# Kernel optimization log

Measured on AMD Instinct MI355X. Metric: run time of the kernel, lower is better.

The kernel has to match this reference:

```python
import jax, jax.numpy as jnp
import numpy as np

N, D, H, O, P = 50000, 256, 512, 64, 1024


def setup_inputs() -> dict:
    key = jax.random.key(0)
    ks = jax.random.split(key, 9)
    x = jax.random.normal(ks[0], (N, D), dtype=jnp.float32)
    W1 = jax.random.normal(ks[1], (H, D), dtype=jnp.float32) / np.sqrt(D)
    b1 = jax.random.normal(ks[2], (H,), dtype=jnp.float32) * 0.01
    W2 = jax.random.normal(ks[3], (O, H), dtype=jnp.float32) / np.sqrt(H)
    b2 = jax.random.normal(ks[4], (O,), dtype=jnp.float32) * 0.01
    ap = jax.random.randint(ks[5], (P,), 0, N, dtype=jnp.int32)
    p = jax.random.randint(ks[6], (P,), 0, N, dtype=jnp.int32)
    an = jax.random.randint(ks[7], (P,), 0, N, dtype=jnp.int32)
    n = jax.random.randint(ks[8], (P,), 0, N, dtype=jnp.int32)
    return {"x": x, "W1": W1, "b1": b1, "W2": W2, "b2": b2,
            "ap": ap, "p": p, "an": an, "n": n}


def reference(x, W1, b1, W2, b2, ap, p, an, n):
    """ContrastiveHessianCalculator.compute_hessian, loss_func='contrastive_full',
    wrt='weight', shape='diagonal', speed='half' (exact GGN diag), for the nnj net
    Linear(D,H) -> Tanh -> Linear(H,O).

    For a pair (x1,x2) the combined diag m0 - 2*m1 + m2 equals
    diag((J1-J2)^T (J1-J2)) where Ji = d f(xi)/d params. Closed form per layer:
      W1[i,j]: S11_i*x1_j^2 - 2*S12_i*x1_j*x2_j + S22_i*x2_j^2,
               Sab_i = tanh'(z1a)_i * tanh'(z1b)_i * sum_o W2[o,i]^2
      b1[i]:   S11_i - 2*S12_i + S22_i
      W2[i,j]: (h1_j - h2_j)^2  (independent of output row i)
      b2[i]:   0  (bias Jacobians of the two branches cancel)
    Per-layer diags are flattened [weight, bias] and concatenated (torch.cat(.., dim=1)),
    then summed over the pair batch; return sum(pos) - sum(neg).
    """
    c = jnp.sum(W2 * W2, axis=0)  # [H]

    def pair_hess_diag(ia, ib):
        xa = x[ia]            # [P, D]
        xb = x[ib]            # [P, D]
        ha = jnp.tanh(xa @ W1.T + b1)   # [P, H]
        hb = jnp.tanh(xb @ W1.T + b1)
        da = 1.0 - ha * ha              # tanh' at x_a, [P, H]
        db = 1.0 - hb * hb
        S11 = da * da * c               # [P, H]
        S12 = da * db * c
        S22 = db * db * c
        # W1 diag: [P, H, D]
        W1d = (S11[:, :, None] * (xa * xa)[:, None, :]
               - 2.0 * S12[:, :, None] * (xa * xb)[:, None, :]
               + S22[:, :, None] * (xb * xb)[:, None, :])
        b1d = S11 - 2.0 * S12 + S22      # [P, H]
        hd = (ha - hb) ** 2              # [P, H]
        W2d = jnp.broadcast_to(hd[:, None, :], (hd.shape[0], O, H))  # [P, O, H]
        b2d = jnp.zeros((hd.shape[0], O), dtype=hd.dtype)
        flat = jnp.concatenate([W1d.reshape(hd.shape[0], -1), b1d,
                                W2d.reshape(hd.shape[0], -1), b2d], axis=1)
        return jnp.sum(flat, axis=0)     # sum over pair batch -> [n_params]

    pos = pair_hess_diag(ap, p)
    neg = pair_hess_diag(an, n)
    return pos - neg
```

## Files before the change

### kernel.cpp

```cpp
#include <hip/hip_runtime.h>
#include <math.h>

#define DD_ 256
#define HH_ 512
#define OO_ 64

typedef __attribute__((ext_vector_type(8))) short bf16x8s;
typedef __attribute__((ext_vector_type(4))) float f32x4;

__device__ __forceinline__ unsigned short f2bf(float f) {
    unsigned u = __float_as_uint(f);
    u += 0x7FFF + ((u >> 16) & 1);
    return (unsigned short)(u >> 16);
}
__device__ __forceinline__ float bf2f(unsigned short h) {
    return __uint_as_float(((unsigned)h) << 16);
}
__device__ __forceinline__ int swz4(int r, int g) {
    return g ^ (r & 3) ^ ((r >> 2) & 3);
}

__global__ __launch_bounds__(256) void k_prep(
    const float* __restrict__ x, const float* __restrict__ W1, const float* __restrict__ W2,
    const int* __restrict__ ap, const int* __restrict__ pI,
    const int* __restrict__ an, const int* __restrict__ nI,
    short* __restrict__ w1hi, short* __restrict__ w1lo,
    float* __restrict__ c, short* __restrict__ Xt) {
    const int t = threadIdx.x;
    const int bb = blockIdx.x;
    if (bb < 128) {
        __shared__ int sia[64], sib[64];
        const int jblk = bb >> 5, pblk = bb & 31;
        const int j = jblk * 64 + (t >> 2), pq = t & 3;
        const int p0 = pblk * 64;
        const int s = p0 >> 10;
        const int* IA = s ? an : ap;
        const int* IB = s ? nI : pI;
        if (t < 64) sia[t] = IA[(p0 & 1023) + t];
        else if (t < 128) sib[t - 64] = IB[(p0 & 1023) + (t - 64)];
        __syncthreads();
        short xv[3][16];
        #pragma unroll
        for (int pp = 0; pp < 16; ++pp) {
            int pl = pq * 16 + pp;
            float xa = x[(size_t)sia[pl] * DD_ + j];
            float xb = x[(size_t)sib[pl] * DD_ + j];
            xv[0][pp] = (short)f2bf(xa * xa);
            xv[1][pp] = (short)f2bf(xa * xb);
            xv[2][pp] = (short)f2bf(xb * xb);
        }
        size_t base = (size_t)j * 6144 + p0 + pq * 16;
        #pragma unroll
        for (int term = 0; term < 3; ++term) {
            bf16x8s v0, v1;
            #pragma unroll
            for (int e = 0; e < 8; ++e) { v0[e] = xv[term][e]; v1[e] = xv[term][e + 8]; }
            *(bf16x8s*)(&Xt[base + (size_t)term * 2048]) = v0;
            *(bf16x8s*)(&Xt[base + (size_t)term * 2048 + 8]) = v1;
        }
    } else if (bb < 144) {
        const int b3 = bb - 128;
        const int r = b3 * 32 + (t >> 3), q = t & 7;
        const float* src = W1 + (size_t)r * DD_ + q * 32;
        const size_t dst = (size_t)r * DD_ + q * 32;
        #pragma unroll
        for (int jj = 0; jj < 4; ++jj) {
            float4 v0 = *(const float4*)(src + jj * 8);
            float4 v1 = *(const float4*)(src + jj * 8 + 4);
            float f[8] = {v0.x, v0.y, v0.z, v0.w, v1.x, v1.y, v1.z, v1.w};
            bf16x8s hi, lo;
            #pragma unroll
            for (int e = 0; e < 8; ++e) {
                unsigned short hh = f2bf(f[e]);
                hi[e] = (short)hh;
                lo[e] = (short)f2bf(f[e] - bf2f(hh));
            }
            *(bf16x8s*)(&w1hi[dst + jj * 8]) = hi;
            *(bf16x8s*)(&w1lo[dst + jj * 8]) = lo;
        }
    } else {
        const int i = (bb - 144) * 256 + t;
        float s = 0.f;
        #pragma unroll
        for (int o = 0; o < OO_; ++o) { float w = W2[o * HH_ + i]; s += w * w; }
        c[i] = s;
    }
}

__global__ __launch_bounds__(256) void k_fused1(
    const float* __restrict__ x,
    const short* __restrict__ w1hi, const short* __restrict__ w1lo,
    const float* __restrict__ b1, const float* __restrict__ c,
    const int* __restrict__ ap, const int* __restrict__ pI,
    const int* __restrict__ an, const int* __restrict__ nI,
    short* __restrict__ Mt, float* __restrict__ pb1, float* __restrict__ phd) {
    __shared__ short Ah[64 * 32], Al[64 * 32], Bh[64 * 32], Bl[64 * 32];
    __shared__ float ht[64][67];
    __shared__ int sidx[64];
    const int t = threadIdx.x;
    const int n0 = blockIdx.x * 64;
    const int ry = blockIdx.y;
    const int s = ry >> 5;
    const int p0 = (ry & 31) * 32;
    const int* IA = s ? an : ap;
    const int* IB = s ? nI : pI;
    if (t < 32) sidx[t] = IA[p0 + t];
    else if (t < 64) sidx[t] = IB[p0 + t - 32];
    __syncthreads();
    const int row = t >> 2, q = t & 3;
    const int l = t & 63, w = t >> 6;
    const int wm = w >> 1, wn = w & 1;
    const int lm = l & 15, g = l >> 4;
    const int sw = swz4(row, q);
    f32x4 acc[2][2] = {};
    for (int k0 = 0; k0 < DD_; k0 += 32) {
        {
            const float* src = x + (size_t)sidx[row] * DD_ + k0 + q * 8;
            float4 v0 = *(const float4*)src;
            float4 v1 = *(const float4*)(src + 4);
            float f[8] = {v0.x, v0.y, v0.z, v0.w, v1.x, v1.y, v1.z, v1.w};
            bf16x8s hi, lo;
            #pragma unroll
            for (int e = 0; e < 8; ++e) {
                unsigned short hh = f2bf(f[e]);
                hi[e] = (short)hh;
                lo[e] = (short)f2bf(f[e] - bf2f(hh));
            }
            *(bf16x8s*)(&Ah[(row * 4 + sw) * 8]) = hi;
            *(bf16x8s*)(&Al[(row * 4 + sw) * 8]) = lo;
        }
        {
            const size_t bsrc = (size_t)(n0 + row) * DD_ + k0 + q * 8;
            *(bf16x8s*)(&Bh[(row * 4 + sw) * 8]) = *(const bf16x8s*)(&w1hi[bsrc]);
            *(bf16x8s*)(&Bl[(row * 4 + sw) * 8]) = *(const bf16x8s*)(&w1lo[bsrc]);
        }
        __syncthreads();
        bf16x8s ah[2], al[2], bh[2], bl[2];
        #pragma unroll
        for (int mi = 0; mi < 2; ++mi) {
            int r = wm * 32 + mi * 16 + lm;
            ah[mi] = *(const bf16x8s*)(&Ah[(r * 4 + swz4(r, g)) * 8]);
            al[mi] = *(const bf16x8s*)(&Al[(r * 4 + swz4(r, g)) * 8]);
        }
        #pragma unroll
        for (int nj = 0; nj < 2; ++nj) {
            int r = wn * 32 + nj * 16 + lm;
            bh[nj] = *(const bf16x8s*)(&Bh[(r * 4 + swz4(r, g)) * 8]);
            bl[nj] = *(const bf16x8s*)(&Bl[(r * 4 + swz4(r, g)) * 8]);
        }
        #pragma unroll
        for (int mi = 0; mi < 2; ++mi)
            #pragma unroll
            for (int nj = 0; nj < 2; ++nj) {
                acc[mi][nj] = __builtin_amdgcn_mfma_f32_16x16x32_bf16(ah[mi], bh[nj], acc[mi][nj], 0, 0, 0);
                acc[mi][nj] = __builtin_amdgcn_mfma_f32_16x16x32_bf16(ah[mi], bl[nj], acc[mi][nj], 0, 0, 0);
                acc[mi][nj] = __builtin_amdgcn_mfma_f32_16x16x32_bf16(al[mi], bh[nj], acc[mi][nj], 0, 0, 0);
            }
        __syncthreads();
    }
    #pragma unroll
    for (int mi = 0; mi < 2; ++mi)
        #pragma unroll
        for (int nj = 0; nj < 2; ++nj) {
            int jl = wn * 32 + nj * 16 + lm;
            float bv = b1[n0 + jl];
            #pragma unroll
            for (int qq = 0; qq < 4; ++qq) {
                int r = wm * 32 + mi * 16 + g * 4 + qq;
                ht[r][jl] = tanhf(acc[mi][nj][qq] + bv);
            }
        }
    __syncthreads();
    const int il = t >> 2, pq = t & 3;
    const float ci = c[n0 + il];
    const float sgn = s ? -1.f : 1.f;
    float b1p = 0.f, hdp = 0.f;
    bf16x8s v0, v1, v2;
    #pragma unroll
    for (int pp = 0; pp < 8; ++pp) {
        int pl = pq * 8 + pp;
        float ha = ht[pl][il];
        float hb = ht[pl + 32][il];
        float da = 1.f - ha * ha, db = 1.f - hb * hb;
        float s11 = sgn * (da * da * ci);
        float s12 = sgn * (-2.f * da * db * ci);
        float s22 = sgn * (db * db * ci);
        v0[pp] = (short)f2bf(s11);
        v1[pp] = (short)f2bf(s12);
        v2[pp] = (short)f2bf(s22);
        b1p += s11 + s12 + s22;
        float d = ha - hb;
        hdp += sgn * d * d;
    }
    size_t base = (size_t)(n0 + il) * 6144 + s * 1024 + p0 + pq * 8;
    *(bf16x8s*)(&Mt[base]) = v0;
    *(bf16x8s*)(&Mt[base + 2048]) = v1;
    *(bf16x8s*)(&Mt[base + 4096]) = v2;
    b1p += __shfl_xor(b1p, 1); b1p += __shfl_xor(b1p, 2);
    hdp += __shfl_xor(hdp, 1); hdp += __shfl_xor(hdp, 2);
    if (pq == 0) { pb1[ry * HH_ + n0 + il] = b1p; phd[ry * HH_ + n0 + il] = hdp; }
}

__global__ __launch_bounds__(256) void k_gemm2(
    const short* __restrict__ Mt, const short* __restrict__ Xt,
    float* __restrict__ part) {
    __shared__ short As[64 * 32], Bs[64 * 32];
    const int t = threadIdx.x;
    const int j0 = blockIdx.x * 64;
    const int i0 = blockIdx.y * 64;
    const int kb = blockIdx.z;
    const int row = t >> 2, q = t & 3;
    const int l = t & 63, w = t >> 6;
    const int wm = w >> 1, wn = w & 1;
    const int lm = l & 15, g = l >> 4;
    const int sw = swz4(row, q);
    f32x4 acc[2][2] = {};
    for (int ks = 0; ks < 12; ++ks) {
        const int k0 = kb * 384 + ks * 32;
        *(bf16x8s*)(&As[(row * 4 + sw) * 8]) =
            *(const bf16x8s*)(&Mt[(size_t)(i0 + row) * 6144 + k0 + q * 8]);
        *(bf16x8s*)(&Bs[(row * 4 + sw) * 8]) =
            *(const bf16x8s*)(&Xt[(size_t)(j0 + row) * 6144 + k0 + q * 8]);
        __syncthreads();
        bf16x8s a[2], b[2];
        #pragma unroll
        for (int mi = 0; mi < 2; ++mi) {
            int r = wm * 32 + mi * 16 + lm;
            a[mi] = *(const bf16x8s*)(&As[(r * 4 + swz4(r, g)) * 8]);
        }
        #pragma unroll
        for (int nj = 0; nj < 2; ++nj) {
            int r = wn * 32 + nj * 16 + lm;
            b[nj] = *(const bf16x8s*)(&Bs[(r * 4 + swz4(r, g)) * 8]);
        }
        #pragma unroll
        for (int mi = 0; mi < 2; ++mi)
            #pragma unroll
            for (int nj = 0; nj < 2; ++nj)
                acc[mi][nj] = __builtin_amdgcn_mfma_f32_16x16x32_bf16(a[mi], b[nj], acc[mi][nj], 0, 0, 0);
        __syncthreads();
    }
    #pragma unroll
    for (int mi = 0; mi < 2; ++mi)
        #pragma unroll
        for (int nj = 0; nj < 2; ++nj) {
            int j = j0 + wn * 32 + nj * 16 + lm;
            #pragma unroll
            for (int qq = 0; qq < 4; ++qq) {
                int i = i0 + wm * 32 + mi * 16 + g * 4 + qq;
                part[((size_t)kb * HH_ + i) * DD_ + j] = acc[mi][nj][qq];
            }
        }
}

__global__ void k_tail(const float* __restrict__ part, const float* __restrict__ pb1,
                       const float* __restrict__ phd, float* __restrict__ out) {
    int gid = blockIdx.x * 256 + threadIdx.x;
    const int HD = HH_ * DD_;
    if (gid < HD) {
        float sv = 0.f;
        #pragma unroll
        for (int kb = 0; kb < 16; ++kb) sv += part[(size_t)kb * HD + gid];
        out[gid] = sv;
    } else if (gid < HD + HH_) {
        int i = gid - HD;
        float sv = 0.f;
        #pragma unroll
        for (int kb = 0; kb < 64; ++kb) sv += pb1[kb * HH_ + i];
        out[gid] = sv;
    } else if (gid < HD + HH_ + OO_ * HH_) {
        int i = (gid - HD - HH_) & (HH_ - 1);
        float sv = 0.f;
        #pragma unroll
        for (int kb = 0; kb < 64; ++kb) sv += phd[kb * HH_ + i];
        out[gid] = sv;
    } else if (gid < HD + HH_ + OO_ * HH_ + OO_) {
        out[gid] = 0.f;
    }
}

extern "C" void kernel_launch(void* const* d_in, const int* in_sizes, int n_in,
                              void* d_out, int out_size, void* d_ws, size_t ws_size,
                              hipStream_t stream) {
    const float* x  = (const float*)d_in[0];
    const float* W1 = (const float*)d_in[1];
    const float* b1 = (const float*)d_in[2];
    const float* W2 = (const float*)d_in[3];
    const int* ap = (const int*)d_in[5];
    const int* pI = (const int*)d_in[6];
    const int* an = (const int*)d_in[7];
    const int* nI = (const int*)d_in[8];
    float* out = (float*)d_out;
    float* ws = (float*)d_ws;

    float* part = ws;
    short* Mt   = (short*)(ws + 2097152);
    short* Xt   = (short*)(ws + 3670016);
    float* pb1  = ws + 4456448;
    float* phd  = ws + 4489216;
    short* w1hi = (short*)(ws + 4521984);
    short* w1lo = (short*)(ws + 4587520);
    float* c    = ws + 4653056;

    k_prep<<<dim3(146), dim3(256), 0, stream>>>(x, W1, W2, ap, pI, an, nI,
                                                w1hi, w1lo, c, Xt);
    k_fused1<<<dim3(8, 64), dim3(256), 0, stream>>>(x, w1hi, w1lo, b1, c,
                                                    ap, pI, an, nI, Mt, pb1, phd);
    k_gemm2<<<dim3(4, 8, 16), dim3(256), 0, stream>>>(Mt, Xt, part);
    k_tail<<<dim3(643), dim3(256), 0, stream>>>(part, pb1, phd, out);
}
```

Before: 36.01 us.

## Merge prep and first GEMM kernels into one launch with inline W1 split

```diff
diff --git a/kernel.cpp b/kernel.cpp
--- a/kernel.cpp
+++ b/kernel.cpp
@@ -20,17 +20,136 @@
     return g ^ (r & 3) ^ ((r >> 2) & 3);
 }
 
-__global__ __launch_bounds__(256) void k_prep(
-    const float* __restrict__ x, const float* __restrict__ W1, const float* __restrict__ W2,
+__global__ __launch_bounds__(256) void k_mega(
+    const float* __restrict__ x, const float* __restrict__ W1,
+    const float* __restrict__ b1, const float* __restrict__ W2,
     const int* __restrict__ ap, const int* __restrict__ pI,
     const int* __restrict__ an, const int* __restrict__ nI,
-    short* __restrict__ w1hi, short* __restrict__ w1lo,
-    float* __restrict__ c, short* __restrict__ Xt) {
+    short* __restrict__ Mt, short* __restrict__ Xt,
+    float* __restrict__ pb1, float* __restrict__ phd) {
     const int t = threadIdx.x;
     const int bb = blockIdx.x;
-    if (bb < 128) {
+    if (bb < 512) {
+        __shared__ short Ah[64 * 32], Al[64 * 32], Bh[64 * 32], Bl[64 * 32];
+        __shared__ float ht[64][67];
+        __shared__ int sidx[64];
+        const int n0 = (bb & 7) * 64;
+        const int ry = bb >> 3;
+        const int s = ry >> 5;
+        const int p0 = (ry & 31) * 32;
+        const int* IA = s ? an : ap;
+        const int* IB = s ? nI : pI;
+        if (t < 32) sidx[t] = IA[p0 + t];
+        else if (t < 64) sidx[t] = IB[p0 + t - 32];
+        __syncthreads();
+        const int row = t >> 2, q = t & 3;
+        const int l = t & 63, w = t >> 6;
+        const int wm = w >> 1, wn = w & 1;
+        const int lm = l & 15, g = l >> 4;
+        const int sw = swz4(row, q);
+        f32x4 acc[2][2] = {};
+        for (int k0 = 0; k0 < DD_; k0 += 32) {
+            {
+                const float* src = x + (size_t)sidx[row] * DD_ + k0 + q * 8;
+                float4 v0 = *(const float4*)src;
+                float4 v1 = *(const float4*)(src + 4);
+                float f[8] = {v0.x, v0.y, v0.z, v0.w, v1.x, v1.y, v1.z, v1.w};
+                bf16x8s hi, lo;
+                #pragma unroll
+                for (int e = 0; e < 8; ++e) {
+                    unsigned short hh = f2bf(f[e]);
+                    hi[e] = (short)hh;
+                    lo[e] = (short)f2bf(f[e] - bf2f(hh));
+                }
+                *(bf16x8s*)(&Ah[(row * 4 + sw) * 8]) = hi;
+                *(bf16x8s*)(&Al[(row * 4 + sw) * 8]) = lo;
+            }
+            {
+                const float* src = W1 + (size_t)(n0 + row) * DD_ + k0 + q * 8;
+                float4 v0 = *(const float4*)src;
+                float4 v1 = *(const float4*)(src + 4);
+                float f[8] = {v0.x, v0.y, v0.z, v0.w, v1.x, v1.y, v1.z, v1.w};
+                bf16x8s hi, lo;
+                #pragma unroll
+                for (int e = 0; e < 8; ++e) {
+                    unsigned short hh = f2bf(f[e]);
+                    hi[e] = (short)hh;
+                    lo[e] = (short)f2bf(f[e] - bf2f(hh));
+                }
+                *(bf16x8s*)(&Bh[(row * 4 + sw) * 8]) = hi;
+                *(bf16x8s*)(&Bl[(row * 4 + sw) * 8]) = lo;
+            }
+            __syncthreads();
+            bf16x8s ah[2], al[2], bh[2], bl[2];
+            #pragma unroll
+            for (int mi = 0; mi < 2; ++mi) {
+                int r = wm * 32 + mi * 16 + lm;
+                ah[mi] = *(const bf16x8s*)(&Ah[(r * 4 + swz4(r, g)) * 8]);
+                al[mi] = *(const bf16x8s*)(&Al[(r * 4 + swz4(r, g)) * 8]);
+            }
+            #pragma unroll
+            for (int nj = 0; nj < 2; ++nj) {
+                int r = wn * 32 + nj * 16 + lm;
+                bh[nj] = *(const bf16x8s*)(&Bh[(r * 4 + swz4(r, g)) * 8]);
+                bl[nj] = *(const bf16x8s*)(&Bl[(r * 4 + swz4(r, g)) * 8]);
+            }
+            #pragma unroll
+            for (int mi = 0; mi < 2; ++mi)
+                #pragma unroll
+                for (int nj = 0; nj < 2; ++nj) {
+                    acc[mi][nj] = __builtin_amdgcn_mfma_f32_16x16x32_bf16(ah[mi], bh[nj], acc[mi][nj], 0, 0, 0);
+                    acc[mi][nj] = __builtin_amdgcn_mfma_f32_16x16x32_bf16(ah[mi], bl[nj], acc[mi][nj], 0, 0, 0);
+                    acc[mi][nj] = __builtin_amdgcn_mfma_f32_16x16x32_bf16(al[mi], bh[nj], acc[mi][nj], 0, 0, 0);
+                }
+            __syncthreads();
+        }
+        #pragma unroll
+        for (int mi = 0; mi < 2; ++mi)
+            #pragma unroll
+            for (int nj = 0; nj < 2; ++nj) {
+                int jl = wn * 32 + nj * 16 + lm;
+                float bv = b1[n0 + jl];
+                #pragma unroll
+                for (int qq = 0; qq < 4; ++qq) {
+                    int r = wm * 32 + mi * 16 + g * 4 + qq;
+                    ht[r][jl] = tanhf(acc[mi][nj][qq] + bv);
+                }
+            }
+        __syncthreads();
+        const int il = t >> 2, pq = t & 3;
+        float ci = 0.f;
+        #pragma unroll 8
+        for (int o = 0; o < OO_; ++o) { float wv = W2[o * HH_ + n0 + il]; ci += wv * wv; }
+        const float sgn = s ? -1.f : 1.f;
+        float b1p = 0.f, hdp = 0.f;
+        bf16x8s v0, v1, v2;
+        #pragma unroll
+        for (int pp = 0; pp < 8; ++pp) {
+            int pl = pq * 8 + pp;
+            float ha = ht[pl][il];
+            float hb = ht[pl + 32][il];
+            float da = 1.f - ha * ha, db = 1.f - hb * hb;
+            float s11 = sgn * (da * da * ci);
+            float s12 = sgn * (-2.f * da * db * ci);
+            float s22 = sgn * (db * db * ci);
+            v0[pp] = (short)f2bf(s11);
+            v1[pp] = (short)f2bf(s12);
+            v2[pp] = (short)f2bf(s22);
+            b1p += s11 + s12 + s22;
+            float d = ha - hb;
+            hdp += sgn * d * d;
+        }
+        size_t base = (size_t)(n0 + il) * 6144 + s * 1024 + p0 + pq * 8;
+        *(bf16x8s*)(&Mt[base]) = v0;
+        *(bf16x8s*)(&Mt[base + 2048]) = v1;
+        *(bf16x8s*)(&Mt[base + 4096]) = v2;
+        b1p += __shfl_xor(b1p, 1); b1p += __shfl_xor(b1p, 2);
+        hdp += __shfl_xor(hdp, 1); hdp += __shfl_xor(hdp, 2);
+        if (pq == 0) { pb1[ry * HH_ + n0 + il] = b1p; phd[ry * HH_ + n0 + il] = hdp; }
+    } else {
         __shared__ int sia[64], sib[64];
-        const int jblk = bb >> 5, pblk = bb & 31;
+        const int b2 = bb - 512;
+        const int jblk = b2 >> 5, pblk = b2 & 31;
         const int j = jblk * 64 + (t >> 2), pq = t & 3;
         const int p0 = pblk * 64;
         const int s = p0 >> 10;
@@ -58,147 +177,7 @@
             *(bf16x8s*)(&Xt[base + (size_t)term * 2048]) = v0;
             *(bf16x8s*)(&Xt[base + (size_t)term * 2048 + 8]) = v1;
         }
-    } else if (bb < 144) {
-        const int b3 = bb - 128;
-        const int r = b3 * 32 + (t >> 3), q = t & 7;
-        const float* src = W1 + (size_t)r * DD_ + q * 32;
-        const size_t dst = (size_t)r * DD_ + q * 32;
-        #pragma unroll
-        for (int jj = 0; jj < 4; ++jj) {
-            float4 v0 = *(const float4*)(src + jj * 8);
-            float4 v1 = *(const float4*)(src + jj * 8 + 4);
-            float f[8] = {v0.x, v0.y, v0.z, v0.w, v1.x, v1.y, v1.z, v1.w};
-            bf16x8s hi, lo;
-            #pragma unroll
-            for (int e = 0; e < 8; ++e) {
-                unsigned short hh = f2bf(f[e]);
-                hi[e] = (short)hh;
-                lo[e] = (short)f2bf(f[e] - bf2f(hh));
-            }
-            *(bf16x8s*)(&w1hi[dst + jj * 8]) = hi;
-            *(bf16x8s*)(&w1lo[dst + jj * 8]) = lo;
-        }
-    } else {
-        const int i = (bb - 144) * 256 + t;
-        float s = 0.f;
-        #pragma unroll
-        for (int o = 0; o < OO_; ++o) { float w = W2[o * HH_ + i]; s += w * w; }
-        c[i] = s;
     }
-}
-
-__global__ __launch_bounds__(256) void k_fused1(
-    const float* __restrict__ x,
-    const short* __restrict__ w1hi, const short* __restrict__ w1lo,
-    const float* __restrict__ b1, const float* __restrict__ c,
-    const int* __restrict__ ap, const int* __restrict__ pI,
-    const int* __restrict__ an, const int* __restrict__ nI,
-    short* __restrict__ Mt, float* __restrict__ pb1, float* __restrict__ phd) {
-    __shared__ short Ah[64 * 32], Al[64 * 32], Bh[64 * 32], Bl[64 * 32];
-    __shared__ float ht[64][67];
-    __shared__ int sidx[64];
-    const int t = threadIdx.x;
-    const int n0 = blockIdx.x * 64;
-    const int ry = blockIdx.y;
-    const int s = ry >> 5;
-    const int p0 = (ry & 31) * 32;
-    const int* IA = s ? an : ap;
-    const int* IB = s ? nI : pI;
-    if (t < 32) sidx[t] = IA[p0 + t];
-    else if (t < 64) sidx[t] = IB[p0 + t - 32];
-    __syncthreads();
-    const int row = t >> 2, q = t & 3;
-    const int l = t & 63, w = t >> 6;
-    const int wm = w >> 1, wn = w & 1;
-    const int lm = l & 15, g = l >> 4;
-    const int sw = swz4(row, q);
-    f32x4 acc[2][2] = {};
-    for (int k0 = 0; k0 < DD_; k0 += 32) {
-        {
-            const float* src = x + (size_t)sidx[row] * DD_ + k0 + q * 8;
-            float4 v0 = *(const float4*)src;
-            float4 v1 = *(const float4*)(src + 4);
-            float f[8] = {v0.x, v0.y, v0.z, v0.w, v1.x, v1.y, v1.z, v1.w};
-            bf16x8s hi, lo;
-            #pragma unroll
-            for (int e = 0; e < 8; ++e) {
-                unsigned short hh = f2bf(f[e]);
-                hi[e] = (short)hh;
-                lo[e] = (short)f2bf(f[e] - bf2f(hh));
-            }
-            *(bf16x8s*)(&Ah[(row * 4 + sw) * 8]) = hi;
-            *(bf16x8s*)(&Al[(row * 4 + sw) * 8]) = lo;
-        }
-        {
-            const size_t bsrc = (size_t)(n0 + row) * DD_ + k0 + q * 8;
-            *(bf16x8s*)(&Bh[(row * 4 + sw) * 8]) = *(const bf16x8s*)(&w1hi[bsrc]);
-            *(bf16x8s*)(&Bl[(row * 4 + sw) * 8]) = *(const bf16x8s*)(&w1lo[bsrc]);
-        }
-        __syncthreads();
-        bf16x8s ah[2], al[2], bh[2], bl[2];
-        #pragma unroll
-        for (int mi = 0; mi < 2; ++mi) {
-            int r = wm * 32 + mi * 16 + lm;
-            ah[mi] = *(const bf16x8s*)(&Ah[(r * 4 + swz4(r, g)) * 8]);
-            al[mi] = *(const bf16x8s*)(&Al[(r * 4 + swz4(r, g)) * 8]);
-        }
-        #pragma unroll
-        for (int nj = 0; nj < 2; ++nj) {
-            int r = wn * 32 + nj * 16 + lm;
-            bh[nj] = *(const bf16x8s*)(&Bh[(r * 4 + swz4(r, g)) * 8]);
-            bl[nj] = *(const bf16x8s*)(&Bl[(r * 4 + swz4(r, g)) * 8]);
-        }
-        #pragma unroll
-        for (int mi = 0; mi < 2; ++mi)
-            #pragma unroll
-            for (int nj = 0; nj < 2; ++nj) {
-                acc[mi][nj] = __builtin_amdgcn_mfma_f32_16x16x32_bf16(ah[mi], bh[nj], acc[mi][nj], 0, 0, 0);
-                acc[mi][nj] = __builtin_amdgcn_mfma_f32_16x16x32_bf16(ah[mi], bl[nj], acc[mi][nj], 0, 0, 0);
-                acc[mi][nj] = __builtin_amdgcn_mfma_f32_16x16x32_bf16(al[mi], bh[nj], acc[mi][nj], 0, 0, 0);
-            }
-        __syncthreads();
-    }
-    #pragma unroll
-    for (int mi = 0; mi < 2; ++mi)
-        #pragma unroll
-        for (int nj = 0; nj < 2; ++nj) {
-            int jl = wn * 32 + nj * 16 + lm;
-            float bv = b1[n0 + jl];
-            #pragma unroll
-            for (int qq = 0; qq < 4; ++qq) {
-                int r = wm * 32 + mi * 16 + g * 4 + qq;
-                ht[r][jl] = tanhf(acc[mi][nj][qq] + bv);
-            }
-        }
-    __syncthreads();
-    const int il = t >> 2, pq = t & 3;
-    const float ci = c[n0 + il];
-    const float sgn = s ? -1.f : 1.f;
-    float b1p = 0.f, hdp = 0.f;
-    bf16x8s v0, v1, v2;
-    #pragma unroll
-    for (int pp = 0; pp < 8; ++pp) {
-        int pl = pq * 8 + pp;
-        float ha = ht[pl][il];
-        float hb = ht[pl + 32][il];
-        float da = 1.f - ha * ha, db = 1.f - hb * hb;
-        float s11 = sgn * (da * da * ci);
-        float s12 = sgn * (-2.f * da * db * ci);
-        float s22 = sgn * (db * db * ci);
-        v0[pp] = (short)f2bf(s11);
-        v1[pp] = (short)f2bf(s12);
-        v2[pp] = (short)f2bf(s22);
-        b1p += s11 + s12 + s22;
-        float d = ha - hb;
-        hdp += sgn * d * d;
-    }
-    size_t base = (size_t)(n0 + il) * 6144 + s * 1024 + p0 + pq * 8;
-    *(bf16x8s*)(&Mt[base]) = v0;
-    *(bf16x8s*)(&Mt[base + 2048]) = v1;
-    *(bf16x8s*)(&Mt[base + 4096]) = v2;
-    b1p += __shfl_xor(b1p, 1); b1p += __shfl_xor(b1p, 2);
-    hdp += __shfl_xor(hdp, 1); hdp += __shfl_xor(hdp, 2);
-    if (pq == 0) { pb1[ry * HH_ + n0 + il] = b1p; phd[ry * HH_ + n0 + il] = hdp; }
 }
 
 __global__ __launch_bounds__(256) void k_gemm2(
@@ -298,14 +277,9 @@
     short* Xt   = (short*)(ws + 3670016);
     float* pb1  = ws + 4456448;
     float* phd  = ws + 4489216;
-    short* w1hi = (short*)(ws + 4521984);
-    short* w1lo = (short*)(ws + 4587520);
-    float* c    = ws + 4653056;
-
-    k_prep<<<dim3(146), dim3(256), 0, stream>>>(x, W1, W2, ap, pI, an, nI,
-                                                w1hi, w1lo, c, Xt);
-    k_fused1<<<dim3(8, 64), dim3(256), 0, stream>>>(x, w1hi, w1lo, b1, c,
-                                                    ap, pI, an, nI, Mt, pb1, phd);
+
+    k_mega<<<dim3(640), dim3(256), 0, stream>>>(x, W1, b1, W2, ap, pI, an, nI,
+                                                Mt, Xt, pb1, phd);
     k_gemm2<<<dim3(4, 8, 16), dim3(256), 0, stream>>>(Mt, Xt, part);
     k_tail<<<dim3(643), dim3(256), 0, stream>>>(part, pb1, phd, out);
 }
```

After: 33.20 us. 7.8% less time.
